# Performance work log

Hardware: AMD Instinct MI355X
Metric: run time of the kernel (lower is better)

## Reference

```python
import jax, jax.numpy as jnp
import numpy as np

B, T, DMODEL, H, DK, DV, FF = 4, 1024, 1024, 16, 64, 64, 4096


def _weight_mask(dmodel, dk):
    # tril ones -> 0 on/below diag, -inf above (matches torch masked_fill)
    m = jnp.tril(jnp.ones((dmodel, dk), dtype=jnp.float32))
    return jnp.where(m == 0, -jnp.inf, 0.0).astype(jnp.float32)


def _mha(Q, K, V, Wq, Wk, Wv, Wo, maskout):
    dk = Wq.shape[-1]
    if maskout:
        mask = _weight_mask(Wq.shape[1], dk)[None]  # (1, dmodel, dk)
        # softmax over the dmodel axis of the masked weight tensors (axis -2)
        Wq = jax.nn.softmax(Wq + mask, axis=-2)
        Wk = jax.nn.softmax(Wk + mask, axis=-2)
    WqQ = jnp.einsum('btd,hdk->bhtk', Q, Wq)
    WkK = jnp.einsum('btd,hdk->bhtk', K, Wk)
    WvV = jnp.einsum('btd,hdv->bhtv', V, Wv)
    scores = jnp.einsum('bhtk,bhsk->bhts', WqQ, WkK) / jnp.sqrt(jnp.float32(dk))
    # NOTE: source softmaxes over axis -2 (the QUERY axis), not the key axis
    attn = jax.nn.softmax(scores, axis=-2)
    out = jnp.einsum('bhts,bhsv->bhtv', attn, WvV)
    b, h, t, dv = out.shape
    out = out.transpose(0, 2, 1, 3).reshape(b, t, h * dv)  # (B, T, dmodel)
    return out @ Wo


def _norm(x):
    mean = jnp.mean(x, axis=-1, keepdims=True)
    std = jnp.std(x, axis=-1, keepdims=True, ddof=1)  # torch.std is unbiased
    return (x - mean) / std


def setup_inputs() -> dict:
    key = jax.random.key(0)
    ks = jax.random.split(key, 14)
    s = 0.02
    return {
        'x': jax.random.normal(ks[0], (B, T, DMODEL), jnp.float32),
        'y': jax.random.normal(ks[1], (B, T, DMODEL), jnp.float32),
        'Wq1': jax.random.normal(ks[2], (H, DMODEL, DK), jnp.float32) * s,
        'Wk1': jax.random.normal(ks[3], (H, DMODEL, DK), jnp.float32) * s,
        'Wv1': jax.random.normal(ks[4], (H, DMODEL, DV), jnp.float32) * s,
        'Wo1': jax.random.normal(ks[5], (DMODEL, DMODEL), jnp.float32) * s,
        'Wq2': jax.random.normal(ks[6], (H, DMODEL, DK), jnp.float32) * s,
        'Wk2': jax.random.normal(ks[7], (H, DMODEL, DK), jnp.float32) * s,
        'Wv2': jax.random.normal(ks[8], (H, DMODEL, DV), jnp.float32) * s,
        'Wo2': jax.random.normal(ks[9], (DMODEL, DMODEL), jnp.float32) * s,
        'w_in': jax.random.normal(ks[10], (FF, DMODEL), jnp.float32) * s,
        'b_in': jax.random.normal(ks[11], (FF,), jnp.float32) * s,
        'w_out': jax.random.normal(ks[12], (DMODEL, FF), jnp.float32) * s,
        'b_out': jax.random.normal(ks[13], (DMODEL,), jnp.float32) * s,
    }


def reference(x, y, Wq1, Wk1, Wv1, Wo1, Wq2, Wk2, Wv2, Wo2, w_in, b_in, w_out, b_out):
    # masked self-attention on decoded seq y
    out1 = _norm(_mha(y, y, y, Wq1, Wk1, Wv1, Wo1, True) + y)
    # cross-attention against encoded seq x
    out2 = _norm(_mha(out1, x, x, Wq2, Wk2, Wv2, Wo2, False) + out1)
    ff = jax.nn.relu(out2 @ w_in.T + b_in) @ w_out.T + b_out
    out3 = _norm(ff + out2)
    return (x, out3)
```

## Files before the change

kernel.cpp:

```cpp
#include <hip/hip_runtime.h>
#include <hip/hip_bf16.h>

#define BB 4
#define TT 1024
#define DD 1024
#define HH 16
#define DKK 64
#define FFF 4096

typedef unsigned short u16;
typedef unsigned int u32;
typedef __attribute__((ext_vector_type(8))) short s16x8;
typedef __attribute__((ext_vector_type(4))) float f32x4;

static __device__ __forceinline__ float bf2f(u16 s) {
  union { u32 u; float f; } v; v.u = ((u32)s) << 16; return v.f;
}
static __device__ __forceinline__ u16 f2bf(float f) {
  union { float f; u32 u; } v; v.f = f;
  u32 r = v.u + 0x7FFFu + ((v.u >> 16) & 1u);
  return (u16)(r >> 16);
}

#define GLDS(gp, lp) __builtin_amdgcn_global_load_lds( \
    (const __attribute__((address_space(1))) u32*)(gp), \
    (__attribute__((address_space(3))) u32*)(lp), 16, 0, 0)

static __device__ __forceinline__ void swz_block(int& bx, int& by) {
  int gx = gridDim.x, gy = gridDim.y;
  int nwg = gx * gy;
  int orig = by * gx + bx;
  int q = nwg >> 3, r = nwg & 7;
  int xcd = orig & 7, sl = orig >> 3;
  int wgid = (xcd < r ? xcd * (q + 1) : r * (q + 1) + (xcd - r) * q) + sl;
  int g = gx << 3;
  int grp = wgid / g, rem = wgid % g;
  bx = rem >> 3;
  by = (grp << 3) + (rem & 7);
}

static __device__ __forceinline__ void swz_attn(int& tileIdx, int& bh) {
  int orig = blockIdx.y * 8 + blockIdx.x;
  int wgid = ((orig & 7) << 6) | (orig >> 3);
  tileIdx = wgid & 7;
  bh = wgid >> 3;
}

__global__ __launch_bounds__(256) void k_prep_all(
    const float* __restrict__ x, float* __restrict__ dout, u16* __restrict__ xb,
    const float* __restrict__ y, u16* __restrict__ yb,
    const float* __restrict__ wi, u16* __restrict__ Wi,
    const float* __restrict__ wo, u16* __restrict__ Wob,
    const float* __restrict__ Wq1, const float* __restrict__ Wk1,
    u16* __restrict__ Bq, u16* __restrict__ Bk,
    const float* __restrict__ Wv1, u16* __restrict__ Bv,
    const float* __restrict__ Wq2, const float* __restrict__ Wk2, const float* __restrict__ Wv2,
    u16* __restrict__ B2,
    const float* __restrict__ Wo1, u16* __restrict__ Bwo1,
    const float* __restrict__ Wo2, u16* __restrict__ Bwo2) {
  __shared__ float red[256];
  __shared__ float t[64][65];
  int bid = blockIdx.x, tid = threadIdx.x;

  if (bid < 128) {
    int idx = bid;
    int sel = idx >> 6;
    int h   = (idx >> 2) & 15;
    int cg  = idx & 3;
    const float* W = sel ? Wk1 : Wq1;
    u16* Bt = sel ? Bk : Bq;
    const float* wh = W + (size_t)h * DD * DKK;
    int c = tid & 15, rg = tid >> 4;
    int k = cg * 16 + c;
    float s0 = 0.f, s1 = 0.f, s2 = 0.f, s3 = 0.f;
    for (int d = rg; d < DD; d += 64) {
      float v0 = wh[(size_t)d * DKK + k];
      float v1 = wh[(size_t)(d + 16) * DKK + k];
      float v2 = wh[(size_t)(d + 32) * DKK + k];
      float v3 = wh[(size_t)(d + 48) * DKK + k];
      if (d      >= k) s0 += __expf(v0);
      if (d + 16 >= k) s1 += __expf(v1);
      if (d + 32 >= k) s2 += __expf(v2);
      if (d + 48 >= k) s3 += __expf(v3);
    }
    red[tid] = (s0 + s1) + (s2 + s3); __syncthreads();
    #pragma unroll
    for (int s = 8; s > 0; s >>= 1) {
      if (rg < s) red[tid] += red[tid + s * 16];
      __syncthreads();
    }
    float rinv = 1.f / red[c];
    u16* orow = Bt + ((size_t)(h * 64 + k)) * DD;
    for (int dd = rg * 64; dd < rg * 64 + 64; dd += 8) {
      u16 ob[8];
      #pragma unroll
      for (int e = 0; e < 8; ++e) {
        int d = dd + e;
        float v = (d >= k) ? __expf(wh[(size_t)d * DKK + k]) * rinv : 0.f;
        ob[e] = f2bf(v);
      }
      *(uint4*)(orow + dd) = *(const uint4*)ob;
    }
    return;
  }

  if (bid < 1152) {
    int idx = bid - 128;
    int zz = idx >> 8; idx &= 255;
    const float* W = (zz == 0) ? Wv1 : ((zz == 1) ? Wq2 : ((zz == 2) ? Wk2 : Wv2));
    u16* Bt = (zz == 0) ? Bv : (B2 + (size_t)(zz - 1) * 1024 * 1024);
    int d0 = (idx & 15) << 6, h = idx >> 4;
    const float* src = W + (size_t)h * DD * DKK + (size_t)d0 * DKK;
    #pragma unroll
    for (int i = 0; i < 16; ++i) {
      int e = i * 256 + tid; int r = e >> 6, c = e & 63;
      t[r][c] = src[(size_t)r * DKK + c];
    }
    __syncthreads();
    #pragma unroll
    for (int it = 0; it < 2; ++it) {
      int e = it * 256 + tid;
      int c = e >> 3, grp = e & 7;
      u16 ob[8];
      #pragma unroll
      for (int j = 0; j < 8; ++j) ob[j] = f2bf(t[grp * 8 + j][c]);
      *(uint4*)(Bt + ((size_t)(h * 64 + c)) * DD + d0 + grp * 8) = *(const uint4*)ob;
    }
    return;
  }

  if (bid < 1664) {
    int idx = bid - 1152;
    int sel = idx >> 8; idx &= 255;
    const float* W = sel ? Wo2 : Wo1;
    u16* Bt = sel ? Bwo2 : Bwo1;
    int k0 = (idx & 15) << 6, n0 = ((idx >> 4) & 15) << 6;
    #pragma unroll
    for (int i = 0; i < 16; ++i) {
      int e = i * 256 + tid; int r = e >> 6, c = e & 63;
      t[r][c] = W[(size_t)(k0 + r) * DD + n0 + c];
    }
    __syncthreads();
    #pragma unroll
    for (int it = 0; it < 2; ++it) {
      int e = it * 256 + tid;
      int c = e >> 3, grp = e & 7;
      u16 ob[8];
      #pragma unroll
      for (int j = 0; j < 8; ++j) ob[j] = f2bf(t[grp * 8 + j][c]);
      *(uint4*)(Bt + (size_t)(n0 + c) * DD + k0 + grp * 8) = *(const uint4*)ob;
    }
    return;
  }

  {
    int idx = bid - 1664;
    int seg = idx >> 12;
    int i = ((idx & 4095) * 256 + tid) * 4;
    if (seg == 0) {
      float4 v = *(const float4*)(x + i);
      *(float4*)(dout + i) = v;
      u16 o[4] = { f2bf(v.x), f2bf(v.y), f2bf(v.z), f2bf(v.w) };
      *(ushort4*)(xb + i) = *(ushort4*)o;
    } else {
      const float* s = (seg == 1) ? y : ((seg == 2) ? wi : wo);
      u16* d = (seg == 1) ? yb : ((seg == 2) ? Wi : Wob);
      float4 v = *(const float4*)(s + i);
      u16 o[4] = { f2bf(v.x), f2bf(v.y), f2bf(v.z), f2bf(v.w) };
      *(ushort4*)(d + i) = *(ushort4*)o;
    }
  }
}

__global__ __launch_bounds__(512) void k_mfma_nt(
    const u16* __restrict__ A, const u16* __restrict__ A2,
    const u16* __restrict__ B,
    u16* __restrict__ P0, u16* __restrict__ P1, u16* __restrict__ P2, u16* __restrict__ P3,
    u16* __restrict__ Cb, u16* __restrict__ Cb2, u16* __restrict__ Ct,
    const float* __restrict__ bias, int relu, int mode, int M, int N, int K) {
  __shared__ u16 SLDS[24576];
  int bx = blockIdx.x, by = blockIdx.y;
  swz_block(bx, by);
  int tid = threadIdx.x, wave = tid >> 6, lane = tid & 63;
  int row0 = by << 7, col0 = bx << 7;
  int wm = (wave >> 2) << 6;
  int wn = (wave & 3) << 5;

  const u16* Asrc = (mode == 1 && A2 && (col0 >> 10) > 0) ? A2 : A;

  int Ksl = K / gridDim.z;
  int kbase = blockIdx.z * Ksl;
  int nt = Ksl >> 5;

  f32x4 acc[4][2];
  #pragma unroll
  for (int m = 0; m < 4; ++m)
    #pragma unroll
    for (int n = 0; n < 2; ++n) acc[m][n] = f32x4{0.f, 0.f, 0.f, 0.f};

  int srow = tid >> 2;
  int scol = ((tid & 3) ^ ((srow >> 1) & 3)) << 3;
  const u16* Ag = Asrc + (size_t)(row0 + srow) * K + scol;
  const u16* Bg = B + (size_t)(col0 + srow) * K + scol;
  int wbase = wave << 9;

  int fr = lane & 15;
  int kg = (((lane >> 4) ^ ((fr >> 1) & 3))) << 3;
  int ardo = (wm + fr) * 32 + kg;
  int brdo = 12288 + (wn + fr) * 32 + kg;

  auto STAGE = [&](int buf, int k0) {
    GLDS(Ag + k0, SLDS + buf * 4096 + wbase);
    GLDS(Bg + k0, SLDS + 12288 + buf * 4096 + wbase);
  };

  STAGE(0, kbase);
  if (nt > 1) STAGE(1, kbase + 32);
  int bufT = 0;
  for (int t = 0; t < nt; ++t) {
    if (t + 1 < nt) asm volatile("s_waitcnt vmcnt(2)" ::: "memory");
    else            asm volatile("s_waitcnt vmcnt(0)" ::: "memory");
    __builtin_amdgcn_s_barrier();
    asm volatile("" ::: "memory");
    if (t + 2 < nt) {
      int b2 = bufT + 2; if (b2 >= 3) b2 -= 3;
      STAGE(b2, kbase + (t + 2) * 32);
    }
    const u16* Ard = SLDS + bufT * 4096 + ardo;
    const u16* Brd = SLDS + bufT * 4096 + brdo;
    s16x8 aF[4], bF[2];
    #pragma unroll
    for (int m = 0; m < 4; ++m) aF[m] = *(const s16x8*)(Ard + m * 16 * 32);
    #pragma unroll
    for (int n = 0; n < 2; ++n) bF[n] = *(const s16x8*)(Brd + n * 16 * 32);
    __builtin_amdgcn_s_setprio(1);
    #pragma unroll
    for (int m = 0; m < 4; ++m)
      #pragma unroll
      for (int n = 0; n < 2; ++n)
        acc[m][n] = __builtin_amdgcn_mfma_f32_16x16x32_bf16(aF[m], bF[n], acc[m][n], 0, 0, 0);
    __builtin_amdgcn_s_setprio(0);
    ++bufT; if (bufT == 3) bufT = 0;
  }
  __syncthreads();

  int fq = (lane >> 4) << 2;

  u16* dstRow = nullptr; u16* dstCol = nullptr;
  int rowPitch = 1024, colBase = col0 & 1023;
  if (mode == 0) {
    rowPitch = N; colBase = col0;
    if (gridDim.z > 1) {
      int z = blockIdx.z;
      dstRow = (z == 0) ? P0 : ((z == 1) ? P1 : ((z == 2) ? P2 : P3));
    } else dstRow = Cb;
  }
  else if (mode == 1) { int q = col0 >> 10; if (q == 0) dstRow = Cb; else if (q == 1) dstRow = Cb2; else dstCol = Ct; }
  else { int q = col0 >> 10; if (q == 0) dstRow = Cb; else dstCol = Ct; }

  u16* Ep = SLDS + wave * 2048;
  #pragma unroll
  for (int m = 0; m < 4; ++m) {
    #pragma unroll
    for (int n = 0; n < 2; ++n) {
      int col = col0 + wn + n * 16 + fr;
      float bs = bias ? bias[col] : 0.f;
      #pragma unroll
      for (int r = 0; r < 4; ++r) {
        float v = acc[m][n][r] + bs;
        if (relu) v = fmaxf(v, 0.f);
        Ep[(fq + r) * 40 + n * 16 + fr] = f2bf(v);
      }
    }
    if (dstRow) {
      int rw = lane >> 2, seg = lane & 3;
      const u16* src = Ep + rw * 40 + seg * 8;
      u16* gd = dstRow + (size_t)(row0 + wm + m * 16 + rw) * rowPitch + colBase + wn + seg * 8;
      *(uint4*)gd = *(const uint4*)src;
    } else {
      int c = lane >> 1, half = lane & 1;
      u16 tmp[8];
      #pragma unroll
      for (int j = 0; j < 8; ++j) tmp[j] = Ep[(half * 8 + j) * 40 + c];
      u16* gd = dstCol + (size_t)(colBase + wn + c) * 4096 + row0 + wm + m * 16 + half * 8;
      *(uint4*)gd = *(const uint4*)tmp;
    }
  }
}

static __device__ __forceinline__ void stage_tile512(const u16* __restrict__ g, int gp, u16* L, int tid) {
  int row = tid >> 3, col8 = (tid & 7) << 3;
  *(uint4*)(L + row * 72 + col8) = *(const uint4*)(g + (size_t)row * gp + col8);
}

__global__ __launch_bounds__(512) void k_attn_stats_mfma(const u16* __restrict__ Qb, const u16* __restrict__ Kb,
                                                         float* __restrict__ csum) {
  __shared__ u16 Ks[2 * 4608];
  __shared__ u16 Qs[4608];
  int tid = threadIdx.x, wave = tid >> 6, lane = tid & 63;
  int tileIdx, bh;
  swz_attn(tileIdx, bh);
  int b = bh >> 4, h = bh & 15;
  int s0 = tileIdx << 7;
  int tile = wave >> 2, sw = wave & 3;
  stage_tile512(Kb + ((size_t)(b * TT + s0)) * DD + h * 64, DD, Ks, tid);
  stage_tile512(Kb + ((size_t)(b * TT + s0 + 64)) * DD + h * 64, DD, Ks + 4608, tid);
  int row = tid >> 3, col8 = (tid & 7) << 3;
  const u16* Qg = Qb + ((size_t)(b * TT) + row) * DD + h * 64 + col8;
  uint4 qreg = *(const uint4*)Qg;
  __syncthreads();
  int fr = lane & 15, g = lane >> 4;
  const u16* Bbase = Ks + tile * 4608 + (sw * 16 + fr) * 72 + g * 8;
  const u16* Abase = Qs + fr * 72 + g * 8;
  s16x8 bF0 = *(const s16x8*)(Bbase);
  s16x8 bF1 = *(const s16x8*)(Bbase + 32);
  float sum = 0.f;
  for (int t0 = 0; t0 < TT; t0 += 64) {
    __syncthreads();
    *(uint4*)(Qs + row * 72 + col8) = qreg;
    __syncthreads();
    if (t0 + 64 < TT) qreg = *(const uint4*)(Qg + (size_t)(t0 + 64) * DD);
    #pragma unroll
    for (int mt = 0; mt < 4; ++mt) {
      f32x4 acc = f32x4{0.f, 0.f, 0.f, 0.f};
      s16x8 a0 = *(const s16x8*)(Abase + mt * 16 * 72);
      s16x8 a1 = *(const s16x8*)(Abase + mt * 16 * 72 + 32);
      acc = __builtin_amdgcn_mfma_f32_16x16x32_bf16(a0, bF0, acc, 0, 0, 0);
      acc = __builtin_amdgcn_mfma_f32_16x16x32_bf16(a1, bF1, acc, 0, 0, 0);
      sum += __expf(acc[0] * 0.125f) + __expf(acc[1] * 0.125f)
           + __expf(acc[2] * 0.125f) + __expf(acc[3] * 0.125f);
    }
  }
  sum += __shfl_xor(sum, 16, 64);
  sum += __shfl_xor(sum, 32, 64);
  if (lane < 16) csum[(size_t)bh * TT + s0 + tile * 64 + sw * 16 + lane] = sum;
}

__global__ __launch_bounds__(512) void k_attn_apply_mfma(const u16* __restrict__ Qb, const u16* __restrict__ Kb,
                                                         const u16* __restrict__ Vt,
                                                         const float* __restrict__ csum,
                                                         u16* __restrict__ Op) {
  __shared__ u16 Qs[2 * 4608];
  __shared__ u16 KV2[2 * 4608];
  __shared__ u16 Pl[8 * 1024];
  __shared__ float rcsL[64];
  u16* Ks = KV2;
  u16* VTs = KV2 + 4608;
  int tid = threadIdx.x, wave = tid >> 6, lane = tid & 63;
  int tileIdx, bh;
  swz_attn(tileIdx, bh);
  int b = bh >> 4, h = bh & 15;
  int t0 = tileIdx << 7;
  int tile = wave >> 2, tw = wave & 3;
  stage_tile512(Qb + ((size_t)(b * TT + t0)) * DD + h * 64, DD, Qs, tid);
  stage_tile512(Qb + ((size_t)(b * TT + t0 + 64)) * DD + h * 64, DD, Qs + 4608, tid);
  int row = tid >> 3, col8 = (tid & 7) << 3;
  const u16* Kg = Kb + ((size_t)(b * TT) + row) * DD + h * 64 + col8;
  const u16* Vg = Vt + ((size_t)(h * 64) + row) * 4096 + (size_t)b * TT + col8;
  const size_t cbase = (size_t)bh * TT;
  uint4 kreg = *(const uint4*)Kg;
  uint4 vreg = *(const uint4*)Vg;
  float rc0 = (tid < 64) ? csum[cbase + tid] : 0.f;
  __syncthreads();
  int fr = lane & 15, g = lane >> 4;
  const u16* QbF = Qs + tile * 4608 + (tw * 16 + fr) * 72 + g * 8;
  const u16* KaF = Ks + fr * 72 + g * 8;
  char* Pw = (char*)(Pl + wave * 1024);
  uint swz = ((uint)(lane & 7)) << 4;
  s16x8 qF0 = *(const s16x8*)(QbF);
  s16x8 qF1 = *(const s16x8*)(QbF + 32);
  f32x4 acc_o[4];
  #pragma unroll
  for (int nt = 0; nt < 4; ++nt) acc_o[nt] = f32x4{0.f, 0.f, 0.f, 0.f};

  for (int s0 = 0; s0 < TT; s0 += 64) {
    __syncthreads();
    *(uint4*)(Ks + row * 72 + col8) = kreg;
    *(uint4*)(VTs + row * 72 + col8) = vreg;
    if (tid < 64) rcsL[tid] = 1.f / rc0;
    __syncthreads();
    if (s0 + 64 < TT) {
      kreg = *(const uint4*)(Kg + (size_t)(s0 + 64) * DD);
      vreg = *(const uint4*)(Vg + s0 + 64);
      if (tid < 64) rc0 = csum[cbase + s0 + 64 + tid];
    }
    #pragma unroll
    for (int mt = 0; mt < 4; ++mt) {
      f32x4 acc = f32x4{0.f, 0.f, 0.f, 0.f};
      s16x8 a0 = *(const s16x8*)(KaF + mt * 16 * 72);
      s16x8 a1 = *(const s16x8*)(KaF + mt * 16 * 72 + 32);
      acc = __builtin_amdgcn_mfma_f32_16x16x32_bf16(a0, qF0, acc, 0, 0, 0);
      acc = __builtin_amdgcn_mfma_f32_16x16x32_bf16(a1, qF1, acc, 0, 0, 0);
      f32x4 rc4 = *(const f32x4*)&rcsL[mt * 16 + g * 4];
      u16 pb[4];
      #pragma unroll
      for (int r = 0; r < 4; ++r)
        pb[r] = f2bf(__expf(acc[r] * 0.125f) * rc4[r]);
      uint woff = (uint)fr * 128 + (uint)(mt * 16 + g * 4) * 2;
      uint2 wv; wv.x = (u32)pb[0] | ((u32)pb[1] << 16); wv.y = (u32)pb[2] | ((u32)pb[3] << 16);
      *(uint2*)(Pw + (woff ^ swz)) = wv;
    }
    uint rbase = (uint)fr * 128;
    s16x8 pF0 = *(const s16x8*)(Pw + ((rbase + g * 16) ^ swz));
    s16x8 pF1 = *(const s16x8*)(Pw + ((rbase + 64 + g * 16) ^ swz));
    #pragma unroll
    for (int nt = 0; nt < 4; ++nt) {
      s16x8 v0 = *(const s16x8*)(VTs + (nt * 16 + fr) * 72 + g * 8);
      s16x8 v1 = *(const s16x8*)(VTs + (nt * 16 + fr) * 72 + 32 + g * 8);
      acc_o[nt] = __builtin_amdgcn_mfma_f32_16x16x32_bf16(pF0, v0, acc_o[nt], 0, 0, 0);
      acc_o[nt] = __builtin_amdgcn_mfma_f32_16x16x32_bf16(pF1, v1, acc_o[nt], 0, 0, 0);
    }
  }
  __syncthreads();
  u16* Ep = KV2 + wave * 1088;
  #pragma unroll
  for (int nt = 0; nt < 4; ++nt)
    #pragma unroll
    for (int r = 0; r < 4; ++r)
      Ep[(g * 4 + r) * 68 + nt * 16 + fr] = f2bf(acc_o[nt][r]);
  {
    int rw = lane >> 2, seg = lane & 3;
    const u16* src = Ep + rw * 68 + seg * 16;
    u16* gd = Op + ((size_t)(b * TT + t0 + tile * 64 + tw * 16 + rw)) * DD + h * 64 + seg * 16;
    #pragma unroll
    for (int i = 0; i < 4; ++i) *(uint2*)(gd + i * 4) = *(const uint2*)(src + i * 4);
  }
}

__global__ __launch_bounds__(256) void k_add_norm(const u16* __restrict__ A, const u16* __restrict__ A2,
                                                  const u16* __restrict__ A3, const u16* __restrict__ A4,
                                                  const float* __restrict__ bias,
                                                  const float* __restrict__ Bv,
                                                  float* __restrict__ O, u16* __restrict__ Ob) {
  int row = blockIdx.x, tid = threadIdx.x;
  size_t base = (size_t)row * DD;
  int c0 = tid * 4;
  __shared__ float red[256];
  float v[4];
  {
    ushort4 a = *(const ushort4*)(A + base + c0);
    float4 bv = *(const float4*)(Bv + base + c0);
    v[0] = bf2f(a.x) + bv.x; v[1] = bf2f(a.y) + bv.y;
    v[2] = bf2f(a.z) + bv.z; v[3] = bf2f(a.w) + bv.w;
  }
  if (A2) {
    ushort4 a = *(const ushort4*)(A2 + base + c0);
    v[0] += bf2f(a.x); v[1] += bf2f(a.y); v[2] += bf2f(a.z); v[3] += bf2f(a.w);
  }
  if (A3) {
    ushort4 a = *(const ushort4*)(A3 + base + c0);
    v[0] += bf2f(a.x); v[1] += bf2f(a.y); v[2] += bf2f(a.z); v[3] += bf2f(a.w);
  }
  if (A4) {
    ushort4 a = *(const ushort4*)(A4 + base + c0);
    v[0] += bf2f(a.x); v[1] += bf2f(a.y); v[2] += bf2f(a.z); v[3] += bf2f(a.w);
  }
  if (bias) {
    float4 bs = *(const float4*)(bias + c0);
    v[0] += bs.x; v[1] += bs.y; v[2] += bs.z; v[3] += bs.w;
  }
  float s = v[0] + v[1] + v[2] + v[3];
  red[tid] = s; __syncthreads();
  for (int t = 128; t > 0; t >>= 1) { if (tid < t) red[tid] += red[tid + t]; __syncthreads(); }
  float mean = red[0] * (1.f / 1024.f);
  __syncthreads();
  float vs = 0.f;
  #pragma unroll
  for (int i = 0; i < 4; ++i) { float d = v[i] - mean; vs += d * d; }
  red[tid] = vs; __syncthreads();
  for (int t = 128; t > 0; t >>= 1) { if (tid < t) red[tid] += red[tid + t]; __syncthreads(); }
  float inv = rsqrtf(red[0] * (1.f / 1023.f));
  float o[4];
  #pragma unroll
  for (int i = 0; i < 4; ++i) o[i] = (v[i] - mean) * inv;
  *(float4*)(O + base + c0) = *(float4*)o;
  if (Ob) {
    u16 ob[4] = { f2bf(o[0]), f2bf(o[1]), f2bf(o[2]), f2bf(o[3]) };
    *(ushort4*)(Ob + base + c0) = *(ushort4*)ob;
  }
}

extern "C" void kernel_launch(void* const* d_in, const int* in_sizes, int n_in,
                              void* d_out, int out_size, void* d_ws, size_t ws_size,
                              hipStream_t stream) {
  (void)in_sizes; (void)n_in; (void)out_size; (void)ws_size;
  const float* x    = (const float*)d_in[0];
  const float* y    = (const float*)d_in[1];
  const float* Wq1  = (const float*)d_in[2];
  const float* Wk1  = (const float*)d_in[3];
  const float* Wv1  = (const float*)d_in[4];
  const float* Wo1  = (const float*)d_in[5];
  const float* Wq2  = (const float*)d_in[6];
  const float* Wk2  = (const float*)d_in[7];
  const float* Wv2  = (const float*)d_in[8];
  const float* Wo2  = (const float*)d_in[9];
  const float* w_in  = (const float*)d_in[10];
  const float* b_in  = (const float*)d_in[11];
  const float* w_out = (const float*)d_in[12];
  const float* b_out = (const float*)d_in[13];

  float* ws = (float*)d_ws;
  size_t off = 0;
  auto allocw = [&](size_t nw) { float* p = ws + off; off += nw; return p; };
  const size_t MR = (size_t)BB * TT;
  const size_t ND = MR * DD;

  u16* Bq   = (u16*)allocw(512 * 1024);
  u16* Bk   = (u16*)allocw(512 * 1024);
  u16* Bv   = (u16*)allocw(512 * 1024);
  u16* Bwo1 = (u16*)allocw(512 * 1024);
  u16* B2   = (u16*)allocw(3 * 512 * 1024);
  u16* Bwo2 = (u16*)allocw(512 * 1024);
  u16* Wi   = (u16*)allocw(2 * 1024 * 1024);
  u16* Wob  = (u16*)allocw(2 * 1024 * 1024);
  u16* xbf  = (u16*)allocw(ND / 2);
  u16* ybf  = (u16*)allocw(ND / 2);
  u16* REG  = (u16*)allocw(ND * 2);
  float* ff2  = allocw(ND);
  float* out1 = allocw(ND);
  float* out2 = allocw(ND);
  float* csum = allocw((size_t)BB * HH * TT);

  u16* Qb = REG;
  u16* Kb = REG + ND;
  u16* Vt = REG + 2 * ND;
  u16* Mb = REG + 3 * ND;
  u16* ff1b = REG;
  u16* out2bf = ybf;
  float* doutHi = (float*)d_out + ND;
  u16* p0 = (u16*)ff2;
  u16* p1 = (u16*)ff2 + ND;
  u16* p2 = (u16*)out1;
  u16* p3 = (u16*)out1 + ND;

  dim3 blk(256), blkG(512), blkA(512);
  dim3 gPrep(18048);
  dim3 gQKV(24, 32);
  dim3 gP2(8, 32, 2);
  dim3 gF1(32, 32);
  dim3 gFF2(8, 32, 4);
  dim3 gAttn(8, 64);
  dim3 gNorm(MR);

  k_prep_all<<<gPrep, blk, 0, stream>>>(x, (float*)d_out, xbf, y, ybf, w_in, Wi, w_out, Wob,
                                        Wq1, Wk1, Bq, Bk, Wv1, Bv,
                                        Wq2, Wk2, Wv2, B2, Wo1, Bwo1, Wo2, Bwo2);

  k_mfma_nt<<<gQKV, blkG, 0, stream>>>(ybf, nullptr, Bq, nullptr, nullptr, nullptr, nullptr, Qb, Kb, Vt, nullptr, 0, 1, 4096, 3072, 1024);
  k_attn_stats_mfma<<<gAttn, blkA, 0, stream>>>(Qb, Kb, csum);
  k_attn_apply_mfma<<<gAttn, blkA, 0, stream>>>(Qb, Kb, Vt, csum, Mb);
  k_mfma_nt<<<gP2, blkG, 0, stream>>>(Mb, nullptr, Bwo1, p0, p1, nullptr, nullptr, nullptr, nullptr, nullptr, nullptr, 0, 0, 4096, 1024, 1024);
  k_add_norm<<<gNorm, blk, 0, stream>>>(p0, p1, nullptr, nullptr, nullptr, y, out1, Mb );

  k_mfma_nt<<<gQKV, blkG, 0, stream>>>(Mb, xbf, B2, nullptr, nullptr, nullptr, nullptr, Qb, Kb, Vt, nullptr, 0, 1, 4096, 3072, 1024);
  k_attn_stats_mfma<<<gAttn, blkA, 0, stream>>>(Qb, Kb, csum);
  k_attn_apply_mfma<<<gAttn, blkA, 0, stream>>>(Qb, Kb, Vt, csum, Mb);
  k_mfma_nt<<<gP2, blkG, 0, stream>>>(Mb, nullptr, Bwo2, p0, p1, nullptr, nullptr, nullptr, nullptr, nullptr, nullptr, 0, 0, 4096, 1024, 1024);
  k_add_norm<<<gNorm, blk, 0, stream>>>(p0, p1, nullptr, nullptr, nullptr, out1, out2, out2bf);

  k_mfma_nt<<<gF1, blkG, 0, stream>>>(out2bf, nullptr, Wi, nullptr, nullptr, nullptr, nullptr, ff1b, nullptr, nullptr, b_in, 1, 0, 4096, 4096, 1024);
  k_mfma_nt<<<gFF2, blkG, 0, stream>>>(ff1b, nullptr, Wob, p0, p1, p2, p3, nullptr, nullptr, nullptr, nullptr, 0, 0, 4096, 1024, 4096);
  k_add_norm<<<gNorm, blk, 0, stream>>>(p0, p1, p2, p3, b_out, out2, doutHi, nullptr);
}
```

Measured before the change: 359.3 us.

## Split prep kernel and overlap second-layer weight conversion with attention stats

The monolithic prep kernel is split. Only the data needed by the first attention block (y, Wq1/Wk1 softmax, Wv1, Wo1) is converted up front. The conversion of x, w_in, w_out, Wq2/Wk2/Wv2 and Wo2 is appended as extra blocks to the first attention-stats launch, so it runs alongside the latency-bound stats work instead of on the critical path. This shortens the serial prep phase, but the stats kernel now has more blocks, more parameters and shares LDS for the transposes, which may disturb its scheduling.

```diff
diff --git a/kernel.cpp b/kernel.cpp
--- a/kernel.cpp
+++ b/kernel.cpp
@@ -46,18 +46,12 @@
   bh = wgid >> 3;
 }
 
-__global__ __launch_bounds__(256) void k_prep_all(
-    const float* __restrict__ x, float* __restrict__ dout, u16* __restrict__ xb,
+__global__ __launch_bounds__(256) void k_prep1(
     const float* __restrict__ y, u16* __restrict__ yb,
-    const float* __restrict__ wi, u16* __restrict__ Wi,
-    const float* __restrict__ wo, u16* __restrict__ Wob,
     const float* __restrict__ Wq1, const float* __restrict__ Wk1,
     u16* __restrict__ Bq, u16* __restrict__ Bk,
     const float* __restrict__ Wv1, u16* __restrict__ Bv,
-    const float* __restrict__ Wq2, const float* __restrict__ Wk2, const float* __restrict__ Wv2,
-    u16* __restrict__ B2,
-    const float* __restrict__ Wo1, u16* __restrict__ Bwo1,
-    const float* __restrict__ Wo2, u16* __restrict__ Bwo2) {
+    const float* __restrict__ Wo1, u16* __restrict__ Bwo1) {
   __shared__ float red[256];
   __shared__ float t[64][65];
   int bid = blockIdx.x, tid = threadIdx.x;
@@ -104,13 +98,10 @@
     return;
   }
 
-  if (bid < 1152) {
+  if (bid < 384) {
     int idx = bid - 128;
-    int zz = idx >> 8; idx &= 255;
-    const float* W = (zz == 0) ? Wv1 : ((zz == 1) ? Wq2 : ((zz == 2) ? Wk2 : Wv2));
-    u16* Bt = (zz == 0) ? Bv : (B2 + (size_t)(zz - 1) * 1024 * 1024);
     int d0 = (idx & 15) << 6, h = idx >> 4;
-    const float* src = W + (size_t)h * DD * DKK + (size_t)d0 * DKK;
+    const float* src = Wv1 + (size_t)h * DD * DKK + (size_t)d0 * DKK;
     #pragma unroll
     for (int i = 0; i < 16; ++i) {
       int e = i * 256 + tid; int r = e >> 6, c = e & 63;
@@ -124,21 +115,18 @@
       u16 ob[8];
       #pragma unroll
       for (int j = 0; j < 8; ++j) ob[j] = f2bf(t[grp * 8 + j][c]);
-      *(uint4*)(Bt + ((size_t)(h * 64 + c)) * DD + d0 + grp * 8) = *(const uint4*)ob;
+      *(uint4*)(Bv + ((size_t)(h * 64 + c)) * DD + d0 + grp * 8) = *(const uint4*)ob;
     }
     return;
   }
 
-  if (bid < 1664) {
-    int idx = bid - 1152;
-    int sel = idx >> 8; idx &= 255;
-    const float* W = sel ? Wo2 : Wo1;
-    u16* Bt = sel ? Bwo2 : Bwo1;
+  if (bid < 640) {
+    int idx = bid - 384;
     int k0 = (idx & 15) << 6, n0 = ((idx >> 4) & 15) << 6;
     #pragma unroll
     for (int i = 0; i < 16; ++i) {
       int e = i * 256 + tid; int r = e >> 6, c = e & 63;
-      t[r][c] = W[(size_t)(k0 + r) * DD + n0 + c];
+      t[r][c] = Wo1[(size_t)(k0 + r) * DD + n0 + c];
     }
     __syncthreads();
     #pragma unroll
@@ -148,27 +136,17 @@
       u16 ob[8];
       #pragma unroll
       for (int j = 0; j < 8; ++j) ob[j] = f2bf(t[grp * 8 + j][c]);
-      *(uint4*)(Bt + (size_t)(n0 + c) * DD + k0 + grp * 8) = *(const uint4*)ob;
+      *(uint4*)(Bwo1 + (size_t)(n0 + c) * DD + k0 + grp * 8) = *(const uint4*)ob;
     }
     return;
   }
 
   {
-    int idx = bid - 1664;
-    int seg = idx >> 12;
-    int i = ((idx & 4095) * 256 + tid) * 4;
-    if (seg == 0) {
-      float4 v = *(const float4*)(x + i);
-      *(float4*)(dout + i) = v;
-      u16 o[4] = { f2bf(v.x), f2bf(v.y), f2bf(v.z), f2bf(v.w) };
-      *(ushort4*)(xb + i) = *(ushort4*)o;
-    } else {
-      const float* s = (seg == 1) ? y : ((seg == 2) ? wi : wo);
-      u16* d = (seg == 1) ? yb : ((seg == 2) ? Wi : Wob);
-      float4 v = *(const float4*)(s + i);
-      u16 o[4] = { f2bf(v.x), f2bf(v.y), f2bf(v.z), f2bf(v.w) };
-      *(ushort4*)(d + i) = *(ushort4*)o;
-    }
+    int idx = bid - 640;
+    int i = (idx * 256 + tid) * 4;
+    float4 v = *(const float4*)(y + i);
+    u16 o[4] = { f2bf(v.x), f2bf(v.y), f2bf(v.z), f2bf(v.w) };
+    *(ushort4*)(yb + i) = *(ushort4*)o;
   }
 }
 
@@ -293,47 +271,117 @@
   *(uint4*)(L + row * 72 + col8) = *(const uint4*)(g + (size_t)row * gp + col8);
 }
 
-__global__ __launch_bounds__(512) void k_attn_stats_mfma(const u16* __restrict__ Qb, const u16* __restrict__ Kb,
-                                                         float* __restrict__ csum) {
+__global__ __launch_bounds__(512) void k_attn_stats_mfma(
+    const u16* __restrict__ Qb, const u16* __restrict__ Kb, float* __restrict__ csum,
+    const float* __restrict__ x, float* __restrict__ dout, u16* __restrict__ xb,
+    const float* __restrict__ wi, u16* __restrict__ Wi,
+    const float* __restrict__ wo, u16* __restrict__ Wob,
+    const float* __restrict__ Wq2, const float* __restrict__ Wk2, const float* __restrict__ Wv2,
+    u16* __restrict__ B2,
+    const float* __restrict__ Wo2, u16* __restrict__ Bwo2) {
   __shared__ u16 Ks[2 * 4608];
   __shared__ u16 Qs[4608];
-  int tid = threadIdx.x, wave = tid >> 6, lane = tid & 63;
-  int tileIdx, bh;
-  swz_attn(tileIdx, bh);
-  int b = bh >> 4, h = bh & 15;
-  int s0 = tileIdx << 7;
-  int tile = wave >> 2, sw = wave & 3;
-  stage_tile512(Kb + ((size_t)(b * TT + s0)) * DD + h * 64, DD, Ks, tid);
-  stage_tile512(Kb + ((size_t)(b * TT + s0 + 64)) * DD + h * 64, DD, Ks + 4608, tid);
-  int row = tid >> 3, col8 = (tid & 7) << 3;
-  const u16* Qg = Qb + ((size_t)(b * TT) + row) * DD + h * 64 + col8;
-  uint4 qreg = *(const uint4*)Qg;
-  __syncthreads();
-  int fr = lane & 15, g = lane >> 4;
-  const u16* Bbase = Ks + tile * 4608 + (sw * 16 + fr) * 72 + g * 8;
-  const u16* Abase = Qs + fr * 72 + g * 8;
-  s16x8 bF0 = *(const s16x8*)(Bbase);
-  s16x8 bF1 = *(const s16x8*)(Bbase + 32);
-  float sum = 0.f;
-  for (int t0 = 0; t0 < TT; t0 += 64) {
+  int bid = blockIdx.x, tid = threadIdx.x;
+
+  if (bid < 512) {
+    int wave = tid >> 6, lane = tid & 63;
+    int wgid = ((bid & 7) << 6) | (bid >> 3);
+    int tileIdx = wgid & 7, bh = wgid >> 3;
+    int b = bh >> 4, h = bh & 15;
+    int s0 = tileIdx << 7;
+    int tile = wave >> 2, sw = wave & 3;
+    stage_tile512(Kb + ((size_t)(b * TT + s0)) * DD + h * 64, DD, Ks, tid);
+    stage_tile512(Kb + ((size_t)(b * TT + s0 + 64)) * DD + h * 64, DD, Ks + 4608, tid);
+    int row = tid >> 3, col8 = (tid & 7) << 3;
+    const u16* Qg = Qb + ((size_t)(b * TT) + row) * DD + h * 64 + col8;
+    uint4 qreg = *(const uint4*)Qg;
     __syncthreads();
-    *(uint4*)(Qs + row * 72 + col8) = qreg;
+    int fr = lane & 15, g = lane >> 4;
+    const u16* Bbase = Ks + tile * 4608 + (sw * 16 + fr) * 72 + g * 8;
+    const u16* Abase = Qs + fr * 72 + g * 8;
+    s16x8 bF0 = *(const s16x8*)(Bbase);
+    s16x8 bF1 = *(const s16x8*)(Bbase + 32);
+    float sum = 0.f;
+    for (int t0 = 0; t0 < TT; t0 += 64) {
+      __syncthreads();
+      *(uint4*)(Qs + row * 72 + col8) = qreg;
+      __syncthreads();
+      if (t0 + 64 < TT) qreg = *(const uint4*)(Qg + (size_t)(t0 + 64) * DD);
+      #pragma unroll
+      for (int mt = 0; mt < 4; ++mt) {
+        f32x4 acc = f32x4{0.f, 0.f, 0.f, 0.f};
+        s16x8 a0 = *(const s16x8*)(Abase + mt * 16 * 72);
+        s16x8 a1 = *(const s16x8*)(Abase + mt * 16 * 72 + 32);
+        acc = __builtin_amdgcn_mfma_f32_16x16x32_bf16(a0, bF0, acc, 0, 0, 0);
+        acc = __builtin_amdgcn_mfma_f32_16x16x32_bf16(a1, bF1, acc, 0, 0, 0);
+        sum += __expf(acc[0] * 0.125f) + __expf(acc[1] * 0.125f)
+             + __expf(acc[2] * 0.125f) + __expf(acc[3] * 0.125f);
+      }
+    }
+    sum += __shfl_xor(sum, 16, 64);
+    sum += __shfl_xor(sum, 32, 64);
+    if (lane < 16) csum[(size_t)bh * TT + s0 + tile * 64 + sw * 16 + lane] = sum;
+    return;
+  }
+
+  int idx = bid - 512;
+  if (idx < 6144) {
+    int seg = idx >> 11;
+    int i = ((idx & 2047) * 512 + tid) * 4;
+    if (seg == 0) {
+      float4 v = *(const float4*)(x + i);
+      *(float4*)(dout + i) = v;
+      u16 o[4] = { f2bf(v.x), f2bf(v.y), f2bf(v.z), f2bf(v.w) };
+      *(ushort4*)(xb + i) = *(ushort4*)o;
+    } else {
+      const float* s = (seg == 1) ? wi : wo;
+      u16* d = (seg == 1) ? Wi : Wob;
+      float4 v = *(const float4*)(s + i);
+      u16 o[4] = { f2bf(v.x), f2bf(v.y), f2bf(v.z), f2bf(v.w) };
+      *(ushort4*)(d + i) = *(ushort4*)o;
+    }
+    return;
+  }
+  idx -= 6144;
+  float* tf = (float*)Ks;
+  if (idx < 768) {
+    int zz = idx >> 8; int ii = idx & 255;
+    const float* W = (zz == 0) ? Wq2 : ((zz == 1) ? Wk2 : Wv2);
+    u16* Bt = B2 + (size_t)zz * 1024 * 1024;
+    int d0 = (ii & 15) << 6, h = ii >> 4;
+    const float* src = W + (size_t)h * DD * DKK + (size_t)d0 * DKK;
+    #pragma unroll
+    for (int i2 = 0; i2 < 8; ++i2) {
+      int e = i2 * 512 + tid; int r = e >> 6, c = e & 63;
+      tf[r * 65 + c] = src[(size_t)r * DKK + c];
+    }
     __syncthreads();
-    if (t0 + 64 < TT) qreg = *(const uint4*)(Qg + (size_t)(t0 + 64) * DD);
-    #pragma unroll
-    for (int mt = 0; mt < 4; ++mt) {
-      f32x4 acc = f32x4{0.f, 0.f, 0.f, 0.f};
-      s16x8 a0 = *(const s16x8*)(Abase + mt * 16 * 72);
-      s16x8 a1 = *(const s16x8*)(Abase + mt * 16 * 72 + 32);
-      acc = __builtin_amdgcn_mfma_f32_16x16x32_bf16(a0, bF0, acc, 0, 0, 0);
-      acc = __builtin_amdgcn_mfma_f32_16x16x32_bf16(a1, bF1, acc, 0, 0, 0);
-      sum += __expf(acc[0] * 0.125f) + __expf(acc[1] * 0.125f)
-           + __expf(acc[2] * 0.125f) + __expf(acc[3] * 0.125f);
-    }
-  }
-  sum += __shfl_xor(sum, 16, 64);
-  sum += __shfl_xor(sum, 32, 64);
-  if (lane < 16) csum[(size_t)bh * TT + s0 + tile * 64 + sw * 16 + lane] = sum;
+    {
+      int c = tid >> 3, grp = tid & 7;
+      u16 ob[8];
+      #pragma unroll
+      for (int j = 0; j < 8; ++j) ob[j] = f2bf(tf[(grp * 8 + j) * 65 + c]);
+      *(uint4*)(Bt + ((size_t)(h * 64 + c)) * DD + d0 + grp * 8) = *(const uint4*)ob;
+    }
+    return;
+  }
+  {
+    int ii = idx - 768;
+    int k0 = (ii & 15) << 6, n0 = ((ii >> 4) & 15) << 6;
+    #pragma unroll
+    for (int i2 = 0; i2 < 8; ++i2) {
+      int e = i2 * 512 + tid; int r = e >> 6, c = e & 63;
+      tf[r * 65 + c] = Wo2[(size_t)(k0 + r) * DD + n0 + c];
+    }
+    __syncthreads();
+    {
+      int c = tid >> 3, grp = tid & 7;
+      u16 ob[8];
+      #pragma unroll
+      for (int j = 0; j < 8; ++j) ob[j] = f2bf(tf[(grp * 8 + j) * 65 + c]);
+      *(uint4*)(Bwo2 + (size_t)(n0 + c) * DD + k0 + grp * 8) = *(const uint4*)ob;
+    }
+  }
 }
 
 __global__ __launch_bounds__(512) void k_attn_apply_mfma(const u16* __restrict__ Qb, const u16* __restrict__ Kb,
@@ -534,7 +582,9 @@
   u16* p3 = (u16*)out1 + ND;
 
   dim3 blk(256), blkG(512), blkA(512);
-  dim3 gPrep(18048);
+  dim3 gPrep1(4736);
+  dim3 gStatsFused(7680);
+  dim3 gStats(512);
   dim3 gQKV(24, 32);
   dim3 gP2(8, 32, 2);
   dim3 gF1(32, 32);
@@ -542,18 +592,18 @@
   dim3 gAttn(8, 64);
   dim3 gNorm(MR);
 
-  k_prep_all<<<gPrep, blk, 0, stream>>>(x, (float*)d_out, xbf, y, ybf, w_in, Wi, w_out, Wob,
-                                        Wq1, Wk1, Bq, Bk, Wv1, Bv,
-                                        Wq2, Wk2, Wv2, B2, Wo1, Bwo1, Wo2, Bwo2);
+  k_prep1<<<gPrep1, blk, 0, stream>>>(y, ybf, Wq1, Wk1, Bq, Bk, Wv1, Bv, Wo1, Bwo1);
 
   k_mfma_nt<<<gQKV, blkG, 0, stream>>>(ybf, nullptr, Bq, nullptr, nullptr, nullptr, nullptr, Qb, Kb, Vt, nullptr, 0, 1, 4096, 3072, 1024);
-  k_attn_stats_mfma<<<gAttn, blkA, 0, stream>>>(Qb, Kb, csum);
+  k_attn_stats_mfma<<<gStatsFused, blkA, 0, stream>>>(Qb, Kb, csum,
+      x, (float*)d_out, xbf, w_in, Wi, w_out, Wob, Wq2, Wk2, Wv2, B2, Wo2, Bwo2);
   k_attn_apply_mfma<<<gAttn, blkA, 0, stream>>>(Qb, Kb, Vt, csum, Mb);
   k_mfma_nt<<<gP2, blkG, 0, stream>>>(Mb, nullptr, Bwo1, p0, p1, nullptr, nullptr, nullptr, nullptr, nullptr, nullptr, 0, 0, 4096, 1024, 1024);
   k_add_norm<<<gNorm, blk, 0, stream>>>(p0, p1, nullptr, nullptr, nullptr, y, out1, Mb );
 
   k_mfma_nt<<<gQKV, blkG, 0, stream>>>(Mb, xbf, B2, nullptr, nullptr, nullptr, nullptr, Qb, Kb, Vt, nullptr, 0, 1, 4096, 3072, 1024);
-  k_attn_stats_mfma<<<gAttn, blkA, 0, stream>>>(Qb, Kb, csum);
+  k_attn_stats_mfma<<<gStats, blkA, 0, stream>>>(Qb, Kb, csum,
+      nullptr, nullptr, nullptr, nullptr, nullptr, nullptr, nullptr, nullptr, nullptr, nullptr, nullptr, nullptr, nullptr);
   k_attn_apply_mfma<<<gAttn, blkA, 0, stream>>>(Qb, Kb, Vt, csum, Mb);
   k_mfma_nt<<<gP2, blkG, 0, stream>>>(Mb, nullptr, Bwo2, p0, p1, nullptr, nullptr, nullptr, nullptr, nullptr, nullptr, 0, 0, 4096, 1024, 1024);
   k_add_norm<<<gNorm, blk, 0, stream>>>(p0, p1, nullptr, nullptr, nullptr, out1, out2, out2bf);
```

New measurement: 363.5 us. No clear change (+1.2%).
